# Optimization experiments

Hardware: AMD Instinct MI355X
Metric: run time of the kernel (lower is better)

## Reference

```python
import jax, jax.numpy as jnp
import numpy as np

BOS = 1
MAX_LEN = 20


def _lstm_cell(x, h, c, Wih, Whh, bih, bhh):
    # torch.nn.LSTMCell gate order: i, f, g, o
    g = x @ Wih.T + h @ Whh.T + bih + bhh
    i, f, gg, o = jnp.split(g, 4, axis=-1)
    c = jax.nn.sigmoid(f) * c + jax.nn.sigmoid(i) * jnp.tanh(gg)
    h = jax.nn.sigmoid(o) * jnp.tanh(c)
    return h, c


def setup_inputs() -> dict:
    key = jax.random.key(0)
    ks = jax.random.split(key, 12)
    B, K, D = 512, 36, 2048
    A, H, Em, V = 512, 512, 300, 10000
    s = 0.02
    rn = lambda k, shape, sc=s: sc * jax.random.normal(k, shape, dtype=jnp.float32)
    return {
        'feats': jax.random.normal(ks[0], (B, K, D), dtype=jnp.float32),
        'Wp': rn(ks[1], (A, D)), 'bp': jnp.zeros((A,), jnp.float32),
        'E': rn(ks[2], (V, Em), 0.1).at[0].set(0.0),  # padding_idx = 0
        'Wih1': rn(ks[3], (4 * H, Em + A)), 'Whh1': rn(ks[4], (4 * H, H)),
        'bih1': jnp.zeros((4 * H,), jnp.float32), 'bhh1': jnp.zeros((4 * H,), jnp.float32),
        'Wih2': rn(ks[5], (4 * H, H + A)), 'Whh2': rn(ks[6], (4 * H, H)),
        'bih2': jnp.zeros((4 * H,), jnp.float32), 'bhh2': jnp.zeros((4 * H,), jnp.float32),
        'Wa1': rn(ks[7], (A, H + A)), 'ba1': jnp.zeros((A,), jnp.float32),
        'wa2': rn(ks[8], (1, A)), 'ba2': jnp.zeros((1,), jnp.float32),
        'Wo': rn(ks[9], (V, H)), 'bo': jnp.zeros((V,), jnp.float32),
    }


def reference(feats, Wp, bp, E, Wih1, Whh1, bih1, bhh1, Wih2, Whh2, bih2, bhh2,
              Wa1, ba1, wa2, ba2, Wo, bo):
    B, K, D = feats.shape
    H = Whh1.shape[1]
    f_att = feats @ Wp.T + bp                      # [B, K, A]
    f_mean = f_att.mean(axis=1)                    # [B, A]
    # attn Linear over concat([h1, f_att]): split columns, precompute f_att term
    Wa1_h, Wa1_f = Wa1[:, :H], Wa1[:, H:]
    att_f = f_att @ Wa1_f.T + ba1                  # [B, K, A]
    x0 = jnp.broadcast_to(E[BOS], (B, E.shape[1]))
    z = jnp.zeros((B, H), jnp.float32)
    carry0 = (x0, z, z, z, z)

    def step(carry, _):
        x, h1, c1, h2, c2 = carry
        h1, c1 = _lstm_cell(jnp.concatenate([x, f_mean], axis=-1), h1, c1,
                            Wih1, Whh1, bih1, bhh1)
        pre = jnp.tanh(att_f + (h1 @ Wa1_h.T)[:, None, :])   # [B, K, A]
        e = pre @ wa2[0] + ba2[0]                            # [B, K]
        alpha = jax.nn.softmax(e, axis=-1)
        ctx = jnp.einsum('bk,bka->ba', alpha, f_att)         # [B, A]
        h2, c2 = _lstm_cell(jnp.concatenate([h1, ctx], axis=-1), h2, c2,
                            Wih2, Whh2, bih2, bhh2)
        logit = h2 @ Wo.T + bo                               # [B, V]  (dropout is identity in eval)
        nxt = jnp.argmax(logit, axis=-1)
        return (E[nxt], h1, c1, h2, c2), nxt

    _, ids = jax.lax.scan(step, carry0, None, length=MAX_LEN - 1)
    return ids.T  # [B, MAX_LEN-1], matches torch.stack(out_ids, 1)
```

## Files before the change

kernel.cpp:

```cpp
#include <hip/hip_runtime.h>
#include <math.h>
#include <stdint.h>

constexpr int Bsz = 512, Kf = 36, Dd = 2048, Aa = 512, Hh = 512, Em = 300;
constexpr int Vv = 10000, TSTEPS = 19, BOS = 1;
constexpr int K1 = 832;
constexpr int K2 = 1536;
constexpr int VvP = 10112;
constexpr int NTL = VvP / 64;
constexpr float SPLIT_S  = 2048.0f;
constexpr float SPLIT_IS = 1.0f / 2048.0f;

#define CDIV(a,b) (((a)+(b)-1)/(b))

typedef _Float16 f16x8 __attribute__((ext_vector_type(8)));
typedef float    f32x4 __attribute__((ext_vector_type(4)));

typedef const unsigned int GU __attribute__((address_space(1)));
typedef unsigned int       LU __attribute__((address_space(3)));

__device__ __forceinline__ void gload16(const void* g, void* l) {
    __builtin_amdgcn_global_load_lds((GU*)g, (LU*)l, 16, 0, 0);
}

template<int N> __device__ __forceinline__ void wait_vm() {
    if constexpr (N == 0)       asm volatile("s_waitcnt vmcnt(0)" ::: "memory");
    else if constexpr (N == 3)  asm volatile("s_waitcnt vmcnt(3)" ::: "memory");
    else if constexpr (N == 6)  asm volatile("s_waitcnt vmcnt(6)" ::: "memory");
    else if constexpr (N == 8)  asm volatile("s_waitcnt vmcnt(8)" ::: "memory");
    else static_assert(N == 0, "unsupported vmcnt literal");
}
#define WAIT_LGKM asm volatile("s_waitcnt lgkmcnt(0)" ::: "memory")
#define SB0 __builtin_amdgcn_sched_barrier(0)
#define BAR __builtin_amdgcn_s_barrier()

__device__ __forceinline__ float sigm(float v) { return 1.0f / (1.0f + expf(-v)); }

__device__ __forceinline__ void wsplit(_Float16* __restrict__ hi, _Float16* __restrict__ lo,
                                       size_t idx, float v) {
    _Float16 h = (_Float16)v;
    hi[idx] = h;
    lo[idx] = (_Float16)((v - (float)h) * SPLIT_S);
}


template<int BM, int BN, int BK, int WVM, int OCC, int EPI>
__global__ __launch_bounds__(256, OCC)
void gemm_sp(const _Float16* __restrict__ Ahi, const _Float16* __restrict__ Alo, int lda,
             const _Float16* __restrict__ Bhi, const _Float16* __restrict__ Blo, int ldb,
             float* __restrict__ C, int ldc, int N, int K,
             const float* __restrict__ bias1, const float* __restrict__ bias2,
             const float* __restrict__ addC,
             float* __restrict__ cbuf,
             _Float16* __restrict__ d1h, _Float16* __restrict__ d1l, int ld1, int off1,
             _Float16* __restrict__ d2h, _Float16* __restrict__ d2l, int ld2, int off2,
             float* __restrict__ candV, int* __restrict__ candI, int ntl)
{
    static_assert(EPI != 2 || WVM == 4, "LSTM epilogue needs 4x1 wave grid");
    constexpr int WVN = 4 / WVM;
    constexpr int WM = BM / WVM, WN = BN / WVN;
    constexpr int MF = WM / 16, NF = WN / 16;
    constexpr int PA  = BK / 8;
    constexpr int PSA = BM * 8 + 8;
    constexpr int PSB = BN * 8 + 8;
    constexpr int SZA = PA * PSA, SZB = PA * PSB;
    constexpr int OAH = 0, OAL = SZA, OBH = 2 * SZA, OBL = 2 * SZA + SZB;
    constexpr int BUF = 2 * SZA + 2 * SZB;
    constexpr int NCHA = BM * BK / 2048;
    constexpr int NCHB = BN * BK / 2048;
    constexpr int LW = 2 * NCHA + 2 * NCHB;
    __shared__ _Float16 sm[2 * BUF];

    const int nt = blockIdx.x, mt = blockIdx.y;
    const int m0 = mt * BM, n0 = nt * BN;

    const int t    = threadIdx.x;
    const int lane = t & 63;
    const int w    = t >> 6;
    const int wr   = w / WVN, wc = w % WVN;
    const int l15  = lane & 15, l4 = lane >> 4;

    f32x4 acch[MF][NF];
    f32x4 accm[MF][NF];
    #pragma unroll
    for (int m = 0; m < MF; ++m)
        #pragma unroll
        for (int n = 0; n < NF; ++n) {
            acch[m][n] = (f32x4){0.f, 0.f, 0.f, 0.f};
            accm[m][n] = (f32x4){0.f, 0.f, 0.f, 0.f};
        }

    const int nkt = K / BK;

    auto stage = [&](int bufo, int kt) {
        #pragma unroll
        for (int i = 0; i < NCHA; ++i) {
            const int q  = i * 256 + t;
            const int p  = q / BM, r = q % BM;
            const int qw = i * 256 + (t & ~63);
            const int pu = qw / BM, ru = qw % BM;
            const size_t goff = (size_t)(m0 + r) * lda + kt * BK + p * 8;
            gload16(Ahi + goff, &sm[bufo + OAH + pu * PSA + ru * 8]);
            gload16(Alo + goff, &sm[bufo + OAL + pu * PSA + ru * 8]);
        }
        #pragma unroll
        for (int i = 0; i < NCHB; ++i) {
            const int q  = i * 256 + t;
            const int p  = q / BN, r = q % BN;
            const int qw = i * 256 + (t & ~63);
            const int pu = qw / BN, ru = qw % BN;
            const size_t goff = (size_t)(n0 + r) * ldb + kt * BK + p * 8;
            gload16(Bhi + goff, &sm[bufo + OBH + pu * PSB + ru * 8]);
            gload16(Blo + goff, &sm[bufo + OBL + pu * PSB + ru * 8]);
// ... 112 lines not shown
                }
        #pragma unroll
        for (int mask = 1; mask < 16; mask <<= 1) {
            #pragma unroll
            for (int m = 0; m < MF; ++m)
                #pragma unroll
                for (int r = 0; r < 4; ++r) {
                    const float ov = __shfl_xor(bv[m][r], mask);
                    const int   oi = __shfl_xor(bix[m][r], mask);
                    if (ov > bv[m][r] || (ov == bv[m][r] && oi < bix[m][r])) {
                        bv[m][r] = ov; bix[m][r] = oi;
                    }
                }
        }
        __syncthreads();
        if (l15 == 0) {
            #pragma unroll
            for (int m = 0; m < MF; ++m)
                #pragma unroll
                for (int r = 0; r < 4; ++r) {
                    const int rl = wr * WM + m * 16 + l4 * 4 + r;
                    sEv[wc * BM + rl] = bv[m][r];
                    sEi[wc * BM + rl] = bix[m][r];
                }
        }
        __syncthreads();
        if (t < BM) {
            float v0 = sEv[t]; int i0 = sEi[t];
            const float v1 = sEv[BM + t]; const int i1 = sEi[BM + t];
            if (v1 > v0 || (v1 == v0 && i1 < i0)) { v0 = v1; i0 = i1; }
            candV[(size_t)(m0 + t) * ntl + nt] = v0;
            candI[(size_t)(m0 + t) * ntl + nt] = i0;
        }
    }
}

__global__ __launch_bounds__(512, 4)
void gemm_af32(const float* __restrict__ Af, int lda,
               const _Float16* __restrict__ Bhi, const _Float16* __restrict__ Blo, int ldb,
               float* __restrict__ C, int ldc, int N, int K,
               const float* __restrict__ bias1, int gxn)
{
    constexpr int BM = 128, BN = 64, BK = 32;
    constexpr int WM = 32, WN = 32;
    constexpr int MF = 2, NF = 2;
    constexpr int PSA = BM * 8 + 8;
    constexpr int PSB = BN * 8 + 8;
    constexpr int PA  = BK / 8;
    constexpr int SZA = PA * PSA, SZB = PA * PSB;
    constexpr int OAH = 0, OAL = SZA, OBH = 2 * SZA, OBL = 2 * SZA + SZB;
    constexpr int BUF = 2 * SZA + 2 * SZB;
    __shared__ _Float16 sm[2 * BUF];

    const int nwg = gridDim.x;
    const int cpx = nwg >> 3;
    const int orig = blockIdx.x;
    const int lid = (orig & 7) * cpx + (orig >> 3);
    const int nt = lid % gxn, mt = lid / gxn;
    const int m0 = mt * BM, n0 = nt * BN;

    const int t    = threadIdx.x;
    const int lane = t & 63;
    const int w    = t >> 6;
    const int wr   = w >> 1, wc = w & 1;
    const int l15  = lane & 15, l4 = lane >> 4;
    const int ar   = t >> 2, ac = t & 3;

    f32x4 acch[MF][NF];
    f32x4 accm[MF][NF];
    #pragma unroll
    for (int m = 0; m < MF; ++m)
        #pragma unroll
        for (int n = 0; n < NF; ++n) {
            acch[m][n] = (f32x4){0.f, 0.f, 0.f, 0.f};
            accm[m][n] = (f32x4){0.f, 0.f, 0.f, 0.f};
        }

    const int nkt = K / BK;

    auto issueA = [&](float4 (&rd)[2], int kt) {
        const float* src = Af + (size_t)(m0 + ar) * lda + kt * BK + ac * 8;
        rd[0] = *(const float4*)src;
        rd[1] = *(const float4*)(src + 4);
    };
    auto writeA = [&](int bufo, float4 (&rd)[2]) {
        const float f[8] = {rd[0].x, rd[0].y, rd[0].z, rd[0].w,
                            rd[1].x, rd[1].y, rd[1].z, rd[1].w};
        f16x8 hi, lo;
        #pragma unroll
        for (int j = 0; j < 8; ++j) {
            _Float16 h = (_Float16)f[j];
            hi[j] = h;
            lo[j] = (_Float16)((f[j] - (float)h) * SPLIT_S);
        }
        *(f16x8*)&sm[bufo + OAH + ac * PSA + ar * 8] = hi;
        *(f16x8*)&sm[bufo + OAL + ac * PSA + ar * 8] = lo;
    };
    auto stageB = [&](int bufo, int kt) {
        const int q = t & 255;
        const int p = q >> 6, r = q & 63;
        const _Float16* src = (t < 256) ? Bhi : Blo;
        const int base = (t < 256) ? (bufo + OBH) : (bufo + OBL);
        const size_t goff = (size_t)(n0 + r) * ldb + kt * BK + p * 8;
        gload16(src + goff, &sm[base + p * PSB + r * 8]);
    };
    auto compute = [&](int bufo) {
        f16x8 ah[MF], al[MF], bh[NF], bl[NF];
        const int pl = l4;
        #pragma unroll
        for (int m = 0; m < MF; ++m) {
            const int row = wr * WM + m * 16 + l15;
            ah[m] = *(const f16x8*)&sm[bufo + OAH + pl * PSA + row * 8];
            al[m] = *(const f16x8*)&sm[bufo + OAL + pl * PSA + row * 8];
        }
        #pragma unroll
        for (int n = 0; n < NF; ++n) {
            const int row = wc * WN + n * 16 + l15;
            bh[n] = *(const f16x8*)&sm[bufo + OBH + pl * PSB + row * 8];
            bl[n] = *(const f16x8*)&sm[bufo + OBL + pl * PSB + row * 8];
        }
        #pragma unroll
        for (int m = 0; m < MF; ++m)
            #pragma unroll
            for (int n = 0; n < NF; ++n) {
                acch[m][n] = __builtin_amdgcn_mfma_f32_16x16x32_f16(ah[m], bh[n], acch[m][n], 0, 0, 0);
                accm[m][n] = __builtin_amdgcn_mfma_f32_16x16x32_f16(ah[m], bl[n], accm[m][n], 0, 0, 0);
                accm[m][n] = __builtin_amdgcn_mfma_f32_16x16x32_f16(al[m], bh[n], accm[m][n], 0, 0, 0);
            }
    };

    float4 rA[2], rB[2];
    issueA(rA, 0); stageB(0, 0);
    for (int kt = 0; kt < nkt; kt += 2) {
        issueA(rB, kt + 1); stageB(BUF, kt + 1);
        wait_vm<3>(); SB0;
        writeA(0, rA);
        WAIT_LGKM; SB0;
        BAR; SB0;
        compute(0);
        SB0; WAIT_LGKM; BAR; SB0;
        if (kt + 2 < nkt) { issueA(rA, kt + 2); stageB(0, kt + 2); wait_vm<3>(); }
        else              { wait_vm<0>(); }
        SB0;
        writeA(BUF, rB);
        WAIT_LGKM; SB0;
        BAR; SB0;
        compute(BUF);
        SB0; WAIT_LGKM; BAR; SB0;
    }

    #pragma unroll
    for (int m = 0; m < MF; ++m) {
        const int rowb = m0 + wr * WM + m * 16 + l4 * 4;
        #pragma unroll
        for (int n = 0; n < NF; ++n) {
            const int col = n0 + wc * WN + n * 16 + l15;
            float bb = bias1 ? bias1[col] : 0.f;
            #pragma unroll
            for (int r = 0; r < 4; ++r) {
                const size_t idx = (size_t)(rowb + r) * ldc + col;
                C[idx] = acch[m][n][r] + accm[m][n][r] * SPLIT_IS + bb;
            }
        }
    }
}

__global__ __launch_bounds__(256)
void split_convert(const float* __restrict__ src, int srcld, int validR,
                   _Float16* __restrict__ dhi, _Float16* __restrict__ dlo,
                   int dstld, int coloff, int R, int C, int gperm)
{
    const int total = R * C;
    for (int i = blockIdx.x * 256 + threadIdx.x; i < total; i += gridDim.x * 256) {
        const int r = i / C, c = i % C;
        int dr = r;
        if (gperm) {
            const int gate = r >> 9, h = r & 511;
            dr = ((h >> 4) << 6) + (gate << 4) + (h & 15);
        }
        const float v = (r < validR) ? src[(size_t)r * srcld + c] : 0.f;
        wsplit(dhi, dlo, (size_t)dr * dstld + coloff + c, v);
    }
}

__global__ __launch_bounds__(256)
void init_kernel(_Float16* __restrict__ a1h0, _Float16* __restrict__ a1l0,
                 _Float16* __restrict__ a1h1, _Float16* __restrict__ a1l1,
                 _Float16* __restrict__ a2h0, _Float16* __restrict__ a2l0,
                 _Float16* __restrict__ a2h1, _Float16* __restrict__ a2l1,
                 float* __restrict__ c1, float* __restrict__ c2,
                 const float* __restrict__ E)
{
    const int idx = blockIdx.x * 256 + threadIdx.x;
    if (idx < Bsz * K1) {
        const int col = idx % K1;
        const float v = (col < Em) ? E[(size_t)BOS * Em + col] : 0.f;
        wsplit(a1h0, a1l0, idx, v);
        wsplit(a1h1, a1l1, idx, 0.f);
    }
    if (idx < Bsz * K2) {
        wsplit(a2h0, a2l0, idx, 0.f);
        wsplit(a2h1, a2l1, idx, 0.f);
    }
    if (idx < Bsz * Hh) { c1[idx] = 0.f; c2[idx] = 0.f; }
}

__global__ __launch_bounds__(256)
void fmean_kernel(const float* __restrict__ f_att, float* __restrict__ f_mean,
                  _Float16* __restrict__ fmh, _Float16* __restrict__ fml)
{
    const int b = blockIdx.x;
    for (int a = threadIdx.x; a < Aa; a += 256) {
        float s = 0.f;
        for (int k = 0; k < Kf; ++k) s += f_att[((size_t)b * Kf + k) * Aa + a];
        const float v = s * (1.0f / 36.0f);
        f_mean[(size_t)b * Aa + a] = v;
        wsplit(fmh, fml, (size_t)b * Aa + a, v);
    }
}

__global__ __launch_bounds__(256)
void attn_fused(const float* __restrict__ att_f, const float* __restrict__ q,
                const float* __restrict__ wa2, const float* __restrict__ ba2,
                const float* __restrict__ f_att,
                _Float16* __restrict__ a2h, _Float16* __restrict__ a2l)
{
    const int b = blockIdx.x, tid = threadIdx.x;
    const int w = tid >> 6, lane = tid & 63;
    __shared__ float se[Kf];
    __shared__ float wk[Kf];
    const float* pq = q + (size_t)b * Aa;
    for (int k = w; k < Kf; k += 4) {
        const float* pf = att_f + ((size_t)b * Kf + k) * Aa;
        float s = 0.f;
        #pragma unroll
        for (int j = 0; j < Aa; j += 64) {
            const int a = j + lane;
            s += tanhf(pf[a] + pq[a]) * wa2[a];
        }
        #pragma unroll
        for (int off = 32; off; off >>= 1) s += __shfl_down(s, off);
        if (lane == 0) se[k] = s + ba2[0];
    }
    __syncthreads();
    if (tid < Kf) {
        float mx = -INFINITY;
        for (int k = 0; k < Kf; ++k) mx = fmaxf(mx, se[k]);
        float ssum = 0.f;
        for (int k = 0; k < Kf; ++k) ssum += expf(se[k] - mx);
        wk[tid] = expf(se[tid] - mx) / ssum;
    }
    __syncthreads();
    for (int a = tid; a < Aa; a += 256) {
        float acc = 0.f;
        for (int k = 0; k < Kf; ++k)
            acc = fmaf(wk[k], f_att[((size_t)b * Kf + k) * Aa + a], acc);
        wsplit(a2h, a2l, (size_t)b * K2 + Hh + a, acc);
    }
}

__global__ __launch_bounds__(256)
void argmax_embed_kernel(const float* __restrict__ candV, const int* __restrict__ candI,
                         const float* __restrict__ E,
                         _Float16* __restrict__ a1h, _Float16* __restrict__ a1l,
                         int* __restrict__ out, int t, int ntl)
{
    const int b = blockIdx.x;
    const int tid = threadIdx.x;
    __shared__ float sv[256];
    __shared__ int   si[256];
    float bvv = -INFINITY; int bii = 0x7fffffff;
    if (tid < ntl) { bvv = candV[(size_t)b * ntl + tid]; bii = candI[(size_t)b * ntl + tid]; }
    sv[tid] = bvv; si[tid] = bii;
    __syncthreads();
    for (int s = 128; s > 0; s >>= 1) {
        if (tid < s) {
            const float v2 = sv[tid + s];
            const int   i2 = si[tid + s];
            if (v2 > sv[tid] || (v2 == sv[tid] && i2 < si[tid])) { sv[tid] = v2; si[tid] = i2; }
        }
        __syncthreads();
    }
    const int idx = si[0];
    if (tid == 0) out[(size_t)b * TSTEPS + t] = idx;
    for (int d = tid; d < Em; d += 256)
        wsplit(a1h, a1l, (size_t)b * K1 + d, E[(size_t)idx * Em + d]);
}

static inline void conv(hipStream_t s, const float* src, int srcld, int validR,
                        _Float16* dhi, _Float16* dlo, int dstld, int coloff,
                        int R, int C, int gperm)
{
    int blocks = CDIV(R * C, 256); if (blocks > 2048) blocks = 2048;
    split_convert<<<dim3(blocks), dim3(256), 0, s>>>(src, srcld, validR, dhi, dlo,
                                                     dstld, coloff, R, C, gperm);
}

extern "C" void kernel_launch(void* const* d_in, const int* in_sizes, int n_in,
                              void* d_out, int out_size, void* d_ws, size_t ws_size,
                              hipStream_t stream)
{
    const float* feats = (const float*)d_in[0];
    const float* Wp    = (const float*)d_in[1];
    const float* bp    = (const float*)d_in[2];
    const float* E     = (const float*)d_in[3];
    const float* Wih1  = (const float*)d_in[4];
    const float* Whh1  = (const float*)d_in[5];
    const float* bih1  = (const float*)d_in[6];
    const float* bhh1  = (const float*)d_in[7];
    const float* Wih2  = (const float*)d_in[8];
    const float* Whh2  = (const float*)d_in[9];
    const float* bih2  = (const float*)d_in[10];
    const float* bhh2  = (const float*)d_in[11];
    const float* Wa1   = (const float*)d_in[12];
    const float* ba1   = (const float*)d_in[13];
    const float* wa2   = (const float*)d_in[14];
    const float* ba2   = (const float*)d_in[15];
    const float* Wo    = (const float*)d_in[16];
    const float* bo    = (const float*)d_in[17];
    int* out = (int*)d_out;
    (void)in_sizes; (void)n_in; (void)out_size; (void)ws_size;

    uint8_t* w = (uint8_t*)d_ws;
    size_t off = 0;
    auto alloc = [&](size_t bytes) { void* p = w + off; off = (off + bytes + 255) & ~(size_t)255; return p; };

    float*     f_att  = (float*)alloc(18432ull * 512 * 4);
    float*     att_f  = (float*)alloc(18432ull * 512 * 4);
    float*     f_mean = (float*)alloc(512ull * 512 * 4);
    _Float16*  fmh    = (_Float16*)alloc(512ull * 512 * 2);
    _Float16*  fml    = (_Float16*)alloc(512ull * 512 * 2);
    _Float16*  wph    = (_Float16*)alloc(512ull * 2048 * 2);
    _Float16*  wpl    = (_Float16*)alloc(512ull * 2048 * 2);
    _Float16*  w1ph   = (_Float16*)alloc(2048ull * K1 * 2);
    _Float16*  w1pl   = (_Float16*)alloc(2048ull * K1 * 2);
    _Float16*  w1ch   = (_Float16*)alloc(2048ull * 512 * 2);
    _Float16*  w1cl   = (_Float16*)alloc(2048ull * 512 * 2);
    _Float16*  w2ph   = (_Float16*)alloc(2048ull * K2 * 2);
    _Float16*  w2pl   = (_Float16*)alloc(2048ull * K2 * 2);
    _Float16*  wahh   = (_Float16*)alloc(512ull * 512 * 2);
    _Float16*  wahl   = (_Float16*)alloc(512ull * 512 * 2);
    _Float16*  wafh   = (_Float16*)alloc(512ull * 512 * 2);
    _Float16*  wafl   = (_Float16*)alloc(512ull * 512 * 2);
    _Float16*  woh    = (_Float16*)alloc((size_t)VvP * 512 * 2);
    _Float16*  wol    = (_Float16*)alloc((size_t)VvP * 512 * 2);
    float*     g1c    = (float*)alloc(512ull * 2048 * 4);
    _Float16*  a1h[2] = {(_Float16*)alloc(512ull * K1 * 2), (_Float16*)alloc(512ull * K1 * 2)};
    _Float16*  a1l[2] = {(_Float16*)alloc(512ull * K1 * 2), (_Float16*)alloc(512ull * K1 * 2)};
    _Float16*  a2h[2] = {(_Float16*)alloc(512ull * K2 * 2), (_Float16*)alloc(512ull * K2 * 2)};
    _Float16*  a2l[2] = {(_Float16*)alloc(512ull * K2 * 2), (_Float16*)alloc(512ull * K2 * 2)};
    float*     c1     = (float*)alloc(512ull * 512 * 4);
    float*     c2     = (float*)alloc(512ull * 512 * 4);
    float*     qbuf   = (float*)alloc(512ull * 512 * 4);
    float*     candV  = (float*)alloc(512ull * NTL * 4);
    int*       candI  = (int*)alloc(512ull * NTL * 4);

    conv(stream, Wp,        Dd,      512,  wph,  wpl,  2048, 0,    512,  2048, 0);
    conv(stream, Wih1,      Em + Aa, 2048, w1ph, w1pl, K1,   0,    2048, Em,   1);
    conv(stream, Whh1,      Hh,      2048, w1ph, w1pl, K1,   Em,   2048, 512,  1);
    conv(stream, Wih1,      Em + Aa, 0,    w1ph, w1pl, K1,   812,  2048, 20,   1);
    conv(stream, Wih1 + Em, Em + Aa, 2048, w1ch, w1cl, 512,  0,    2048, 512,  1);
    conv(stream, Wih2,      Hh + Aa, 2048, w2ph, w2pl, K2,   0,    2048, 1024, 1);
    conv(stream, Whh2,      Hh,      2048, w2ph, w2pl, K2,   1024, 2048, 512,  1);
    conv(stream, Wa1,       Hh + Aa, 512,  wahh, wahl, 512,  0,    512,  512,  0);
    conv(stream, Wa1 + Hh,  Hh + Aa, 512,  wafh, wafl, 512,  0,    512,  512,  0);
    conv(stream, Wo,        Hh,      Vv,   woh,  wol,  512,  0,    VvP,  512,  0);

    init_kernel<<<dim3(CDIV(Bsz * K2, 256)), dim3(256), 0, stream>>>(
        a1h[0], a1l[0], a1h[1], a1l[1], a2h[0], a2l[0], a2h[1], a2l[1], c1, c2, E);

    gemm_af32<<<dim3(1152), dim3(512), 0, stream>>>(
        feats, Dd, wph, wpl, 2048, f_att, 512, 512, 2048, bp, 8);
    fmean_kernel<<<dim3(Bsz), dim3(256), 0, stream>>>(f_att, f_mean, fmh, fml);
    gemm_sp<64, 64, 64, 2, 1, 1><<<dim3(32, 8), 256, 0, stream>>>(
        fmh, fml, 512, w1ch, w1cl, 512, g1c, 2048, 2048, 512,
        bih1, bhh1, nullptr,
        nullptr, nullptr, nullptr, 0, 0, nullptr, nullptr, 0, 0, nullptr, nullptr, 0);
    gemm_af32<<<dim3(1152), dim3(512), 0, stream>>>(
        f_att, 512, wafh, wafl, 512, att_f, 512, 512, 512, ba1, 8);

    for (int t = 0; t < TSTEPS; ++t) {
        const int cur = t & 1, nxt = cur ^ 1;
        gemm_sp<64, 64, 64, 4, 2, 2><<<dim3(32, 8), 256, 0, stream>>>(
            a1h[cur], a1l[cur], K1, w1ph, w1pl, K1, nullptr, 2048, 2048, K1,
            nullptr, nullptr, g1c,
            c1, a2h[cur], a2l[cur], K2, 0, a1h[nxt], a1l[nxt], K1, Em,
            nullptr, nullptr, 0);
        gemm_sp<64, 64, 64, 2, 1, 0><<<dim3(8, 8), 256, 0, stream>>>(
            a2h[cur], a2l[cur], K2, wahh, wahl, 512, qbuf, 512, 512, 512,
            nullptr, nullptr, nullptr,
            nullptr, nullptr, nullptr, 0, 0, nullptr, nullptr, 0, 0, nullptr, nullptr, 0);
        attn_fused<<<dim3(Bsz), dim3(256), 0, stream>>>(
            att_f, qbuf, wa2, ba2, f_att, a2h[cur], a2l[cur]);
        gemm_sp<64, 64, 64, 4, 2, 2><<<dim3(32, 8), 256, 0, stream>>>(
            a2h[cur], a2l[cur], K2, w2ph, w2pl, K2, nullptr, 2048, 2048, K2,
            bih2, bhh2, nullptr,
            c2, a2h[nxt], a2l[nxt], K2, 1024, nullptr, nullptr, 0, 0,
            nullptr, nullptr, 0);
        gemm_sp<64, 64, 64, 2, 1, 3><<<dim3(NTL, 8), 256, 0, stream>>>(
            a2h[nxt] + 1024, a2l[nxt] + 1024, K2, woh, wol, 512, nullptr, 0, Vv, 512,
            bo, nullptr, nullptr,
            nullptr, nullptr, nullptr, 0, 0, nullptr, nullptr, 0, 0, candV, candI, NTL);
        argmax_embed_kernel<<<dim3(Bsz), dim3(256), 0, stream>>>(
            candV, candI, E, a1h[nxt], a1l[nxt], out, t, NTL);
    }
}
```

Baseline: 3.394 ms.

## Fuse decode loop into one persistent kernel with software grid barriers

Replaces the 19×6 per-step kernel launches with a single persistent kernel of 512 blocks that runs every decode stage and separates stages with an atomic-counter grid barrier. The aim is to remove launch and inter-kernel gap overhead across the many small serial steps. In exchange, the barriers cost spinning and atomics, only part of the blocks work in some stages, and correctness relies on all 512 blocks being co-resident (launch bounds allow 2 per CU). Occupancy is also capped by the shared-memory and launch-bounds settings.

```diff
diff --git a/kernel.cpp b/kernel.cpp
--- a/kernel.cpp
+++ b/kernel.cpp
@@ -8,6 +8,7 @@
 constexpr int K2 = 1536;
 constexpr int VvP = 10112;
 constexpr int NTL = VvP / 64;
+constexpr int NBLK = 512;
 constexpr float SPLIT_S  = 2048.0f;
 constexpr float SPLIT_IS = 1.0f / 2048.0f;
 
@@ -44,17 +45,40 @@
 }
 
 
-template<int BM, int BN, int BK, int WVM, int OCC, int EPI>
-__global__ __launch_bounds__(256, OCC)
-void gemm_sp(const _Float16* __restrict__ Ahi, const _Float16* __restrict__ Alo, int lda,
-             const _Float16* __restrict__ Bhi, const _Float16* __restrict__ Blo, int ldb,
-             float* __restrict__ C, int ldc, int N, int K,
-             const float* __restrict__ bias1, const float* __restrict__ bias2,
-             const float* __restrict__ addC,
-             float* __restrict__ cbuf,
-             _Float16* __restrict__ d1h, _Float16* __restrict__ d1l, int ld1, int off1,
-             _Float16* __restrict__ d2h, _Float16* __restrict__ d2l, int ld2, int off2,
-             float* __restrict__ candV, int* __restrict__ candI, int ntl)
+constexpr int SMEM64 = 2 * (2 * 8 * (64 * 8 + 8) + 2 * 8 * (64 * 8 + 8));
+
+__device__ __forceinline__ void gbar(unsigned* cnt, unsigned* sns, unsigned& ls) {
+    __syncthreads();
+    if (threadIdx.x == 0) {
+        const unsigned next = ls + 1;
+        __threadfence();
+        const unsigned prev = __hip_atomic_fetch_add(cnt, 1u, __ATOMIC_ACQ_REL,
+                                                     __HIP_MEMORY_SCOPE_AGENT);
+        if (prev == (unsigned)NBLK - 1) {
+            __hip_atomic_store(cnt, 0u, __ATOMIC_RELAXED, __HIP_MEMORY_SCOPE_AGENT);
+            __hip_atomic_store(sns, next, __ATOMIC_RELEASE, __HIP_MEMORY_SCOPE_AGENT);
+        } else {
+            while (__hip_atomic_load(sns, __ATOMIC_ACQUIRE,
+                                     __HIP_MEMORY_SCOPE_AGENT) < next)
+                __builtin_amdgcn_s_sleep(8);
+        }
+        ls = next;
+    }
+    __syncthreads();
+}
+
+template<int BM, int BN, int BK, int WVM, int EPI>
+__device__ void gemm_dev(
+    _Float16* __restrict__ sm, int mt, int nt,
+    const _Float16* __restrict__ Ahi, const _Float16* __restrict__ Alo, int lda,
+    const _Float16* __restrict__ Bhi, const _Float16* __restrict__ Blo, int ldb,
+    float* __restrict__ C, int ldc, int N, int K,
+    const float* __restrict__ bias1, const float* __restrict__ bias2,
+    const float* __restrict__ addC,
+    float* __restrict__ cbuf,
+    _Float16* __restrict__ d1h, _Float16* __restrict__ d1l, int ld1, int off1,
+    _Float16* __restrict__ d2h, _Float16* __restrict__ d2l, int ld2, int off2,
+    float* __restrict__ candV, int* __restrict__ candI, int ntl)
 {
     static_assert(EPI != 2 || WVM == 4, "LSTM epilogue needs 4x1 wave grid");
     constexpr int WVN = 4 / WVM;
@@ -69,16 +93,15 @@
     constexpr int NCHA = BM * BK / 2048;
     constexpr int NCHB = BN * BK / 2048;
     constexpr int LW = 2 * NCHA + 2 * NCHB;
-    __shared__ _Float16 sm[2 * BUF];
-
-    const int nt = blockIdx.x, mt = blockIdx.y;
+
     const int m0 = mt * BM, n0 = nt * BN;
-
     const int t    = threadIdx.x;
     const int lane = t & 63;
     const int w    = t >> 6;
     const int wr   = w / WVN, wc = w % WVN;
     const int l15  = lane & 15, l4 = lane >> 4;
+
+    __syncthreads();
 
     f32x4 acch[MF][NF];
     f32x4 accm[MF][NF];
@@ -260,6 +283,152 @@
     }
 }
 
+template<int BM, int BN, int BK, int WVM, int EPI>
+__global__ __launch_bounds__(256, 2)
+void gemm16(const _Float16* __restrict__ Ahi, const _Float16* __restrict__ Alo, int lda,
+            const _Float16* __restrict__ Bhi, const _Float16* __restrict__ Blo, int ldb,
+            float* __restrict__ C, int ldc, int N, int K,
+            const float* __restrict__ bias1, const float* __restrict__ bias2)
+{
+    __shared__ _Float16 sm[SMEM64];
+    gemm_dev<BM, BN, BK, WVM, EPI>(sm, blockIdx.y, blockIdx.x,
+        Ahi, Alo, lda, Bhi, Blo, ldb, C, ldc, N, K,
+        bias1, bias2, nullptr,
+        nullptr, nullptr, nullptr, 0, 0, nullptr, nullptr, 0, 0,
+        nullptr, nullptr, 0);
+}
+
+__device__ void attn_dev(_Float16* smbase, int b,
+                         const float* __restrict__ att_f, const float* __restrict__ q,
+                         const float* __restrict__ wa2, const float* __restrict__ ba2,
+                         const float* __restrict__ f_att,
+                         _Float16* __restrict__ a2h, _Float16* __restrict__ a2l)
+{
+    float* se = reinterpret_cast<float*>(smbase);
+    float* wk = se + Kf;
+    const int tid = threadIdx.x;
+    const int w = tid >> 6, lane = tid & 63;
+    __syncthreads();
+    const float* pq = q + (size_t)b * Aa;
+    for (int k = w; k < Kf; k += 4) {
+        const float* pf = att_f + ((size_t)b * Kf + k) * Aa;
+        float s = 0.f;
+        #pragma unroll
+        for (int j = 0; j < Aa; j += 64) {
+            const int a = j + lane;
+            s += tanhf(pf[a] + pq[a]) * wa2[a];
+        }
+        #pragma unroll
+        for (int off = 32; off; off >>= 1) s += __shfl_down(s, off);
+        if (lane == 0) se[k] = s + ba2[0];
+    }
+    __syncthreads();
+    if (tid < Kf) {
+        float mx = -INFINITY;
+        for (int k = 0; k < Kf; ++k) mx = fmaxf(mx, se[k]);
+        float ssum = 0.f;
+        for (int k = 0; k < Kf; ++k) ssum += expf(se[k] - mx);
+        wk[tid] = expf(se[tid] - mx) / ssum;
+    }
+    __syncthreads();
+    for (int a = tid; a < Aa; a += 256) {
+        float acc = 0.f;
+        for (int k = 0; k < Kf; ++k)
+            acc = fmaf(wk[k], f_att[((size_t)b * Kf + k) * Aa + a], acc);
+        wsplit(a2h, a2l, (size_t)b * K2 + Hh + a, acc);
+    }
+}
+
+__device__ void argmax_dev(_Float16* smbase, int b,
+                           const float* __restrict__ candV, const int* __restrict__ candI,
+                           const float* __restrict__ E,
+                           _Float16* __restrict__ a1h, _Float16* __restrict__ a1l,
+                           int* __restrict__ out, int t, int ntl)
+{
+    float* sv = reinterpret_cast<float*>(smbase);
+    int*   si = reinterpret_cast<int*>(sv + 256);
+    const int tid = threadIdx.x;
+    __syncthreads();
+    float bvv = -INFINITY; int bii = 0x7fffffff;
+    if (tid < ntl) { bvv = candV[(size_t)b * ntl + tid]; bii = candI[(size_t)b * ntl + tid]; }
+    sv[tid] = bvv; si[tid] = bii;
+    __syncthreads();
+    for (int s = 128; s > 0; s >>= 1) {
+        if (tid < s) {
+            const float v2 = sv[tid + s];
+            const int   i2 = si[tid + s];
+            if (v2 > sv[tid] || (v2 == sv[tid] && i2 < si[tid])) { sv[tid] = v2; si[tid] = i2; }
+        }
+        __syncthreads();
+    }
+    const int idx = si[0];
+    if (tid == 0) out[(size_t)b * TSTEPS + t] = idx;
+    for (int d = tid; d < Em; d += 256)
+        wsplit(a1h, a1l, (size_t)b * K1 + d, E[(size_t)idx * Em + d]);
+}
+
+struct DecodeArgs {
+    _Float16 *a1h0, *a1l0, *a1h1, *a1l1;
+    _Float16 *a2h0, *a2l0, *a2h1, *a2l1;
+    const _Float16 *w1ph, *w1pl, *w2ph, *w2pl, *wahh, *wahl, *woh, *wol;
+    const float *g1c, *bih2, *bhh2, *bo, *wa2, *ba2, *att_f, *f_att, *E;
+    float *c1, *c2, *qbuf, *candV;
+    int *candI, *outp;
+    unsigned *barCnt, *barSns;
+};
+
+__global__ __launch_bounds__(256, 2)
+void decode_loop(DecodeArgs A)
+{
+    __shared__ _Float16 sm[SMEM64];
+    const int blk = blockIdx.x;
+    unsigned ls = 0;
+    _Float16* a1h[2] = {A.a1h0, A.a1h1};
+    _Float16* a1l[2] = {A.a1l0, A.a1l1};
+    _Float16* a2h[2] = {A.a2h0, A.a2h1};
+    _Float16* a2l[2] = {A.a2l0, A.a2l1};
+
+    for (int t = 0; t < TSTEPS; ++t) {
+        const int cur = t & 1, nxt = cur ^ 1;
+        if (blk < 256)
+            gemm_dev<64, 64, 64, 4, 2>(sm, blk >> 5, blk & 31,
+                a1h[cur], a1l[cur], K1, A.w1ph, A.w1pl, K1,
+                nullptr, 2048, 2048, K1,
+                nullptr, nullptr, A.g1c,
+                A.c1, a2h[cur], a2l[cur], K2, 0, a1h[nxt], a1l[nxt], K1, Em,
+                nullptr, nullptr, 0);
+        gbar(A.barCnt, A.barSns, ls);
+        if (blk < 64)
+            gemm_dev<64, 64, 64, 2, 0>(sm, blk >> 3, blk & 7,
+                a2h[cur], a2l[cur], K2, A.wahh, A.wahl, 512,
+                A.qbuf, 512, 512, 512,
+                nullptr, nullptr, nullptr,
+                nullptr, nullptr, nullptr, 0, 0, nullptr, nullptr, 0, 0,
+                nullptr, nullptr, 0);
+        gbar(A.barCnt, A.barSns, ls);
+        attn_dev(sm, blk, A.att_f, A.qbuf, A.wa2, A.ba2, A.f_att, a2h[cur], a2l[cur]);
+        gbar(A.barCnt, A.barSns, ls);
+        if (blk < 256)
+            gemm_dev<64, 64, 64, 4, 2>(sm, blk >> 5, blk & 31,
+                a2h[cur], a2l[cur], K2, A.w2ph, A.w2pl, K2,
+                nullptr, 2048, 2048, K2,
+                A.bih2, A.bhh2, nullptr,
+                A.c2, a2h[nxt], a2l[nxt], K2, 1024, nullptr, nullptr, 0, 0,
+                nullptr, nullptr, 0);
+        gbar(A.barCnt, A.barSns, ls);
+        for (int j = blk; j < 8 * NTL; j += NBLK)
+            gemm_dev<64, 64, 64, 2, 3>(sm, j / NTL, j % NTL,
+                a2h[nxt] + 1024, a2l[nxt] + 1024, K2, A.woh, A.wol, 512,
+                nullptr, 0, Vv, 512,
+                A.bo, nullptr, nullptr,
+                nullptr, nullptr, nullptr, 0, 0, nullptr, nullptr, 0, 0,
+                A.candV, A.candI, NTL);
+        gbar(A.barCnt, A.barSns, ls);
+        argmax_dev(sm, blk, A.candV, A.candI, A.E, a1h[nxt], a1l[nxt], A.outp, t, NTL);
+        gbar(A.barCnt, A.barSns, ls);
+    }
+}
+
 __global__ __launch_bounds__(512, 4)
 void gemm_af32(const float* __restrict__ Af, int lda,
                const _Float16* __restrict__ Bhi, const _Float16* __restrict__ Blo, int ldb,
@@ -414,6 +583,7 @@
                  _Float16* __restrict__ a2h0, _Float16* __restrict__ a2l0,
                  _Float16* __restrict__ a2h1, _Float16* __restrict__ a2l1,
                  float* __restrict__ c1, float* __restrict__ c2,
+                 unsigned* __restrict__ bar,
                  const float* __restrict__ E)
 {
     const int idx = blockIdx.x * 256 + threadIdx.x;
@@ -428,6 +598,7 @@
         wsplit(a2h1, a2l1, idx, 0.f);
     }
     if (idx < Bsz * Hh) { c1[idx] = 0.f; c2[idx] = 0.f; }
+    if (idx < 2) bar[idx] = 0u;
 }
 
 __global__ __launch_bounds__(256)
@@ -442,74 +613,6 @@
         f_mean[(size_t)b * Aa + a] = v;
         wsplit(fmh, fml, (size_t)b * Aa + a, v);
     }
-}
-
-__global__ __launch_bounds__(256)
-void attn_fused(const float* __restrict__ att_f, const float* __restrict__ q,
-                const float* __restrict__ wa2, const float* __restrict__ ba2,
-                const float* __restrict__ f_att,
-                _Float16* __restrict__ a2h, _Float16* __restrict__ a2l)
-{
-    const int b = blockIdx.x, tid = threadIdx.x;
-    const int w = tid >> 6, lane = tid & 63;
-    __shared__ float se[Kf];
-    __shared__ float wk[Kf];
-    const float* pq = q + (size_t)b * Aa;
-    for (int k = w; k < Kf; k += 4) {
-        const float* pf = att_f + ((size_t)b * Kf + k) * Aa;
-        float s = 0.f;
-        #pragma unroll
-        for (int j = 0; j < Aa; j += 64) {
-            const int a = j + lane;
-            s += tanhf(pf[a] + pq[a]) * wa2[a];
-        }
-        #pragma unroll
-        for (int off = 32; off; off >>= 1) s += __shfl_down(s, off);
-        if (lane == 0) se[k] = s + ba2[0];
-    }
-    __syncthreads();
-    if (tid < Kf) {
-        float mx = -INFINITY;
-        for (int k = 0; k < Kf; ++k) mx = fmaxf(mx, se[k]);
-        float ssum = 0.f;
-        for (int k = 0; k < Kf; ++k) ssum += expf(se[k] - mx);
-        wk[tid] = expf(se[tid] - mx) / ssum;
-    }
-    __syncthreads();
-    for (int a = tid; a < Aa; a += 256) {
-        float acc = 0.f;
-        for (int k = 0; k < Kf; ++k)
-            acc = fmaf(wk[k], f_att[((size_t)b * Kf + k) * Aa + a], acc);
-        wsplit(a2h, a2l, (size_t)b * K2 + Hh + a, acc);
-    }
-}
-
-__global__ __launch_bounds__(256)
-void argmax_embed_kernel(const float* __restrict__ candV, const int* __restrict__ candI,
-                         const float* __restrict__ E,
-                         _Float16* __restrict__ a1h, _Float16* __restrict__ a1l,
-                         int* __restrict__ out, int t, int ntl)
-{
-    const int b = blockIdx.x;
-    const int tid = threadIdx.x;
-    __shared__ float sv[256];
-    __shared__ int   si[256];
-    float bvv = -INFINITY; int bii = 0x7fffffff;
-    if (tid < ntl) { bvv = candV[(size_t)b * ntl + tid]; bii = candI[(size_t)b * ntl + tid]; }
-    sv[tid] = bvv; si[tid] = bii;
-    __syncthreads();
-    for (int s = 128; s > 0; s >>= 1) {
-        if (tid < s) {
-            const float v2 = sv[tid + s];
-            const int   i2 = si[tid + s];
-            if (v2 > sv[tid] || (v2 == sv[tid] && i2 < si[tid])) { sv[tid] = v2; si[tid] = i2; }
-        }
-        __syncthreads();
-    }
-    const int idx = si[0];
-    if (tid == 0) out[(size_t)b * TSTEPS + t] = idx;
-    for (int d = tid; d < Em; d += 256)
-        wsplit(a1h, a1l, (size_t)b * K1 + d, E[(size_t)idx * Em + d]);
 }
 
 static inline void conv(hipStream_t s, const float* src, int srcld, int validR,
@@ -579,6 +682,7 @@
     float*     qbuf   = (float*)alloc(512ull * 512 * 4);
     float*     candV  = (float*)alloc(512ull * NTL * 4);
     int*       candI  = (int*)alloc(512ull * NTL * 4);
+    unsigned*  barSt  = (unsigned*)alloc(256);
 
     conv(stream, Wp,        Dd,      512,  wph,  wpl,  2048, 0,    512,  2048, 0);
     conv(stream, Wih1,      Em + Aa, 2048, w1ph, w1pl, K1,   0,    2048, Em,   1);
@@ -592,41 +696,26 @@
     conv(stream, Wo,        Hh,      Vv,   woh,  wol,  512,  0,    VvP,  512,  0);
 
     init_kernel<<<dim3(CDIV(Bsz * K2, 256)), dim3(256), 0, stream>>>(
-        a1h[0], a1l[0], a1h[1], a1l[1], a2h[0], a2l[0], a2h[1], a2l[1], c1, c2, E);
+        a1h[0], a1l[0], a1h[1], a1l[1], a2h[0], a2l[0], a2h[1], a2l[1],
+        c1, c2, barSt, E);
 
     gemm_af32<<<dim3(1152), dim3(512), 0, stream>>>(
         feats, Dd, wph, wpl, 2048, f_att, 512, 512, 2048, bp, 8);
     fmean_kernel<<<dim3(Bsz), dim3(256), 0, stream>>>(f_att, f_mean, fmh, fml);
-    gemm_sp<64, 64, 64, 2, 1, 1><<<dim3(32, 8), 256, 0, stream>>>(
-        fmh, fml, 512, w1ch, w1cl, 512, g1c, 2048, 2048, 512,
-        bih1, bhh1, nullptr,
-        nullptr, nullptr, nullptr, 0, 0, nullptr, nullptr, 0, 0, nullptr, nullptr, 0);
+    gemm16<64, 64, 64, 2, 1><<<dim3(32, 8), 256, 0, stream>>>(
+        fmh, fml, 512, w1ch, w1cl, 512, g1c, 2048, 2048, 512, bih1, bhh1);
     gemm_af32<<<dim3(1152), dim3(512), 0, stream>>>(
         f_att, 512, wafh, wafl, 512, att_f, 512, 512, 512, ba1, 8);
 
-    for (int t = 0; t < TSTEPS; ++t) {
-        const int cur = t & 1, nxt = cur ^ 1;
-        gemm_sp<64, 64, 64, 4, 2, 2><<<dim3(32, 8), 256, 0, stream>>>(
-            a1h[cur], a1l[cur], K1, w1ph, w1pl, K1, nullptr, 2048, 2048, K1,
-            nullptr, nullptr, g1c,
-            c1, a2h[cur], a2l[cur], K2, 0, a1h[nxt], a1l[nxt], K1, Em,
-            nullptr, nullptr, 0);
-        gemm_sp<64, 64, 64, 2, 1, 0><<<dim3(8, 8), 256, 0, stream>>>(
-            a2h[cur], a2l[cur], K2, wahh, wahl, 512, qbuf, 512, 512, 512,
-            nullptr, nullptr, nullptr,
-            nullptr, nullptr, nullptr, 0, 0, nullptr, nullptr, 0, 0, nullptr, nullptr, 0);
-        attn_fused<<<dim3(Bsz), dim3(256), 0, stream>>>(
-            att_f, qbuf, wa2, ba2, f_att, a2h[cur], a2l[cur]);
-        gemm_sp<64, 64, 64, 4, 2, 2><<<dim3(32, 8), 256, 0, stream>>>(
-            a2h[cur], a2l[cur], K2, w2ph, w2pl, K2, nullptr, 2048, 2048, K2,
-            bih2, bhh2, nullptr,
-            c2, a2h[nxt], a2l[nxt], K2, 1024, nullptr, nullptr, 0, 0,
-            nullptr, nullptr, 0);
-        gemm_sp<64, 64, 64, 2, 1, 3><<<dim3(NTL, 8), 256, 0, stream>>>(
-            a2h[nxt] + 1024, a2l[nxt] + 1024, K2, woh, wol, 512, nullptr, 0, Vv, 512,
-            bo, nullptr, nullptr,
-            nullptr, nullptr, nullptr, 0, 0, nullptr, nullptr, 0, 0, candV, candI, NTL);
-        argmax_embed_kernel<<<dim3(Bsz), dim3(256), 0, stream>>>(
-            candV, candI, E, a1h[nxt], a1l[nxt], out, t, NTL);
-    }
-}
+    DecodeArgs da;
+    da.a1h0 = a1h[0]; da.a1l0 = a1l[0]; da.a1h1 = a1h[1]; da.a1l1 = a1l[1];
+    da.a2h0 = a2h[0]; da.a2l0 = a2l[0]; da.a2h1 = a2h[1]; da.a2l1 = a2l[1];
+    da.w1ph = w1ph; da.w1pl = w1pl; da.w2ph = w2ph; da.w2pl = w2pl;
+    da.wahh = wahh; da.wahl = wahl; da.woh = woh; da.wol = wol;
+    da.g1c = g1c; da.bih2 = bih2; da.bhh2 = bhh2; da.bo = bo;
+    da.wa2 = wa2; da.ba2 = ba2; da.att_f = att_f; da.f_att = f_att; da.E = E;
+    da.c1 = c1; da.c2 = c2; da.qbuf = qbuf; da.candV = candV;
+    da.candI = candI; da.outp = out;
+    da.barCnt = barSt; da.barSns = barSt + 1;
+    decode_loop<<<dim3(NBLK), dim3(256), 0, stream>>>(da);
+}
```

After: 13.32 ms. +292.4%, slower.

## Fuse final argmax and embedding lookup into vocab GEMM via last-block counter

Applied to the files above, without the earlier changes.

Drops the separate argmax_embed kernel. The vocab-projection GEMM now uses an atomic per-row-tile counter, so the last finishing block reduces the candidate maxima, writes the output ids, and scatters the split-fp16 embeddings for the next step. This removes one launch per timestep and the associated tail bubble, at the cost of a serialized reduction in a single block per row tile plus a threadfence and atomic in every block. It also raises gemm_af32 launch-bounds occupancy from 4 to 6.

```diff
diff --git a/kernel.cpp b/kernel.cpp
--- a/kernel.cpp
+++ b/kernel.cpp
@@ -54,7 +54,9 @@
              float* __restrict__ cbuf,
              _Float16* __restrict__ d1h, _Float16* __restrict__ d1l, int ld1, int off1,
              _Float16* __restrict__ d2h, _Float16* __restrict__ d2l, int ld2, int off2,
-             float* __restrict__ candV, int* __restrict__ candI, int ntl)
+             float* __restrict__ candV, int* __restrict__ candI, int ntl,
+             unsigned* __restrict__ cnt, const float* __restrict__ Eemb,
+             int* __restrict__ outp, int tstep)
 {
     static_assert(EPI != 2 || WVM == 4, "LSTM epilogue needs 4x1 wave grid");
     constexpr int WVN = 4 / WVM;
@@ -257,10 +259,54 @@
             candV[(size_t)(m0 + t) * ntl + nt] = v0;
             candI[(size_t)(m0 + t) * ntl + nt] = i0;
         }
-    }
-}
-
-__global__ __launch_bounds__(512, 4)
+        __threadfence();
+        __syncthreads();
+        __shared__ int sDone;
+        if (t == 0) {
+            const unsigned prev = __hip_atomic_fetch_add(cnt + mt, 1u,
+                                    __ATOMIC_ACQ_REL, __HIP_MEMORY_SCOPE_AGENT);
+            sDone = (prev == (unsigned)ntl - 1);
+            if (sDone) __hip_atomic_store(cnt + mt, 0u, __ATOMIC_RELAXED,
+                                          __HIP_MEMORY_SCOPE_AGENT);
+        }
+        __syncthreads();
+        if (!sDone) return;
+        float* sV = reinterpret_cast<float*>(&sm[0]);
+        int*   sI = reinterpret_cast<int*>(sV + 256);
+        int*   sIdx = sI + 256;
+        const int rl = t & 63, part = t >> 6;
+        const int b = m0 + rl;
+        float fv = -INFINITY; int fi = 0x7fffffff;
+        const int j0 = part * ((ntl + 3) >> 2);
+        const int j1 = min(ntl, j0 + ((ntl + 3) >> 2));
+        for (int j = j0; j < j1; ++j) {
+            const float v2 = candV[(size_t)b * ntl + j];
+            const int   i2 = candI[(size_t)b * ntl + j];
+            if (v2 > fv || (v2 == fv && i2 < fi)) { fv = v2; fi = i2; }
+        }
+        sV[t] = fv; sI[t] = fi;
+        __syncthreads();
+        if (t < 64) {
+            float v0 = sV[t]; int i0 = sI[t];
+            #pragma unroll
+            for (int p2 = 1; p2 < 4; ++p2) {
+                const float v2 = sV[t + p2 * 64];
+                const int   i2 = sI[t + p2 * 64];
+                if (v2 > v0 || (v2 == v0 && i2 < i0)) { v0 = v2; i0 = i2; }
+            }
+            outp[(size_t)(m0 + t) * TSTEPS + tstep] = i0;
+            sIdx[t] = i0;
+        }
+        __syncthreads();
+        for (int i = t; i < 64 * Em; i += 256) {
+            const int bb = i / Em, d = i % Em;
+            wsplit(d1h, d1l, (size_t)(m0 + bb) * ld1 + d,
+                   Eemb[(size_t)sIdx[bb] * Em + d]);
+        }
+    }
+}
+
+__global__ __launch_bounds__(512, 6)
 void gemm_af32(const float* __restrict__ Af, int lda,
                const _Float16* __restrict__ Bhi, const _Float16* __restrict__ Blo, int ldb,
                float* __restrict__ C, int ldc, int N, int K,
@@ -414,6 +460,7 @@
                  _Float16* __restrict__ a2h0, _Float16* __restrict__ a2l0,
                  _Float16* __restrict__ a2h1, _Float16* __restrict__ a2l1,
                  float* __restrict__ c1, float* __restrict__ c2,
+                 unsigned* __restrict__ cnt,
                  const float* __restrict__ E)
 {
     const int idx = blockIdx.x * 256 + threadIdx.x;
@@ -428,6 +475,7 @@
         wsplit(a2h1, a2l1, idx, 0.f);
     }
     if (idx < Bsz * Hh) { c1[idx] = 0.f; c2[idx] = 0.f; }
+    if (idx < 8) cnt[idx] = 0u;
 }
 
 __global__ __launch_bounds__(256)
@@ -482,34 +530,6 @@
             acc = fmaf(wk[k], f_att[((size_t)b * Kf + k) * Aa + a], acc);
         wsplit(a2h, a2l, (size_t)b * K2 + Hh + a, acc);
     }
-}
-
-__global__ __launch_bounds__(256)
-void argmax_embed_kernel(const float* __restrict__ candV, const int* __restrict__ candI,
-                         const float* __restrict__ E,
-                         _Float16* __restrict__ a1h, _Float16* __restrict__ a1l,
-                         int* __restrict__ out, int t, int ntl)
-{
-    const int b = blockIdx.x;
-    const int tid = threadIdx.x;
-    __shared__ float sv[256];
-    __shared__ int   si[256];
-    float bvv = -INFINITY; int bii = 0x7fffffff;
-    if (tid < ntl) { bvv = candV[(size_t)b * ntl + tid]; bii = candI[(size_t)b * ntl + tid]; }
-    sv[tid] = bvv; si[tid] = bii;
-    __syncthreads();
-    for (int s = 128; s > 0; s >>= 1) {
-        if (tid < s) {
-            const float v2 = sv[tid + s];
-            const int   i2 = si[tid + s];
-            if (v2 > sv[tid] || (v2 == sv[tid] && i2 < si[tid])) { sv[tid] = v2; si[tid] = i2; }
-        }
-        __syncthreads();
-    }
-    const int idx = si[0];
-    if (tid == 0) out[(size_t)b * TSTEPS + t] = idx;
-    for (int d = tid; d < Em; d += 256)
-        wsplit(a1h, a1l, (size_t)b * K1 + d, E[(size_t)idx * Em + d]);
 }
 
 static inline void conv(hipStream_t s, const float* src, int srcld, int validR,
@@ -579,6 +599,7 @@
     float*     qbuf   = (float*)alloc(512ull * 512 * 4);
     float*     candV  = (float*)alloc(512ull * NTL * 4);
     int*       candI  = (int*)alloc(512ull * NTL * 4);
+    unsigned*  cntArr = (unsigned*)alloc(256);
 
     conv(stream, Wp,        Dd,      512,  wph,  wpl,  2048, 0,    512,  2048, 0);
     conv(stream, Wih1,      Em + Aa, 2048, w1ph, w1pl, K1,   0,    2048, Em,   1);
@@ -592,7 +613,8 @@
     conv(stream, Wo,        Hh,      Vv,   woh,  wol,  512,  0,    VvP,  512,  0);
 
     init_kernel<<<dim3(CDIV(Bsz * K2, 256)), dim3(256), 0, stream>>>(
-        a1h[0], a1l[0], a1h[1], a1l[1], a2h[0], a2l[0], a2h[1], a2l[1], c1, c2, E);
+        a1h[0], a1l[0], a1h[1], a1l[1], a2h[0], a2l[0], a2h[1], a2l[1],
+        c1, c2, cntArr, E);
 
     gemm_af32<<<dim3(1152), dim3(512), 0, stream>>>(
         feats, Dd, wph, wpl, 2048, f_att, 512, 512, 2048, bp, 8);
@@ -600,7 +622,8 @@
     gemm_sp<64, 64, 64, 2, 1, 1><<<dim3(32, 8), 256, 0, stream>>>(
         fmh, fml, 512, w1ch, w1cl, 512, g1c, 2048, 2048, 512,
         bih1, bhh1, nullptr,
-        nullptr, nullptr, nullptr, 0, 0, nullptr, nullptr, 0, 0, nullptr, nullptr, 0);
+        nullptr, nullptr, nullptr, 0, 0, nullptr, nullptr, 0, 0,
+        nullptr, nullptr, 0, nullptr, nullptr, nullptr, 0);
     gemm_af32<<<dim3(1152), dim3(512), 0, stream>>>(
         f_att, 512, wafh, wafl, 512, att_f, 512, 512, 512, ba1, 8);
 
@@ -610,23 +633,23 @@
             a1h[cur], a1l[cur], K1, w1ph, w1pl, K1, nullptr, 2048, 2048, K1,
             nullptr, nullptr, g1c,
             c1, a2h[cur], a2l[cur], K2, 0, a1h[nxt], a1l[nxt], K1, Em,
-            nullptr, nullptr, 0);
+            nullptr, nullptr, 0, nullptr, nullptr, nullptr, 0);
         gemm_sp<64, 64, 64, 2, 1, 0><<<dim3(8, 8), 256, 0, stream>>>(
             a2h[cur], a2l[cur], K2, wahh, wahl, 512, qbuf, 512, 512, 512,
             nullptr, nullptr, nullptr,
-            nullptr, nullptr, nullptr, 0, 0, nullptr, nullptr, 0, 0, nullptr, nullptr, 0);
+            nullptr, nullptr, nullptr, 0, 0, nullptr, nullptr, 0, 0,
+            nullptr, nullptr, 0, nullptr, nullptr, nullptr, 0);
         attn_fused<<<dim3(Bsz), dim3(256), 0, stream>>>(
             att_f, qbuf, wa2, ba2, f_att, a2h[cur], a2l[cur]);
         gemm_sp<64, 64, 64, 4, 2, 2><<<dim3(32, 8), 256, 0, stream>>>(
             a2h[cur], a2l[cur], K2, w2ph, w2pl, K2, nullptr, 2048, 2048, K2,
             bih2, bhh2, nullptr,
             c2, a2h[nxt], a2l[nxt], K2, 1024, nullptr, nullptr, 0, 0,
-            nullptr, nullptr, 0);
+            nullptr, nullptr, 0, nullptr, nullptr, nullptr, 0);
         gemm_sp<64, 64, 64, 2, 1, 3><<<dim3(NTL, 8), 256, 0, stream>>>(
             a2h[nxt] + 1024, a2l[nxt] + 1024, K2, woh, wol, 512, nullptr, 0, Vv, 512,
             bo, nullptr, nullptr,
-            nullptr, nullptr, nullptr, 0, 0, nullptr, nullptr, 0, 0, candV, candI, NTL);
-        argmax_embed_kernel<<<dim3(Bsz), dim3(256), 0, stream>>>(
-            candV, candI, E, a1h[nxt], a1l[nxt], out, t, NTL);
-    }
-}
+            nullptr, a1h[nxt], a1l[nxt], K1, 0, nullptr, nullptr, 0, 0,
+            candV, candI, NTL, cntArr, E, out, t);
+    }
+}
```

Measured after the change: 6.956 ms. +105.0%, slower.

## Pre-split feats into fp16 hi/lo and stage A via async LDS loads

Applied to the files above, without the earlier changes.

Adds a separate pass that splits the fp32 feats tensor into fp16 hi/lo arrays, and makes the big projection GEMM load both A halves with direct global-to-LDS loads instead of register loads with in-kernel conversion. The first GEMM also writes a hi/lo split of f_att, so the second GEMM reads pre-split input. The goal is to remove register staging and conversion from the GEMM main loop and simplify its pipeline. The cost is an extra full pass over feats plus fp16 traffic: reading 151MB of fp32 and writing 151MB of fp16, then reading that 151MB back in the GEMM, versus reading 151MB once before.

```diff
diff --git a/kernel.cpp b/kernel.cpp
--- a/kernel.cpp
+++ b/kernel.cpp
@@ -260,11 +260,13 @@
     }
 }
 
+template<int PAIR>
 __global__ __launch_bounds__(512, 4)
-void gemm_af32(const float* __restrict__ Af, int lda,
-               const _Float16* __restrict__ Bhi, const _Float16* __restrict__ Blo, int ldb,
-               float* __restrict__ C, int ldc, int N, int K,
-               const float* __restrict__ bias1, int gxn)
+void gemm_sp512(const _Float16* __restrict__ Ahi, const _Float16* __restrict__ Alo, int lda,
+                const _Float16* __restrict__ Bhi, const _Float16* __restrict__ Blo, int ldb,
+                float* __restrict__ C, int ldc, int N, int K,
+                const float* __restrict__ bias1, int gxn,
+                _Float16* __restrict__ pairH, _Float16* __restrict__ pairL)
 {
     constexpr int BM = 128, BN = 64, BK = 32;
     constexpr int WM = 32, WN = 32;
@@ -289,7 +291,6 @@
     const int w    = t >> 6;
     const int wr   = w >> 1, wc = w & 1;
     const int l15  = lane & 15, l4 = lane >> 4;
-    const int ar   = t >> 2, ac = t & 3;
 
     f32x4 acch[MF][NF];
     f32x4 accm[MF][NF];
@@ -303,31 +304,21 @@
 
     const int nkt = K / BK;
 
-    auto issueA = [&](float4 (&rd)[2], int kt) {
-        const float* src = Af + (size_t)(m0 + ar) * lda + kt * BK + ac * 8;
-        rd[0] = *(const float4*)src;
-        rd[1] = *(const float4*)(src + 4);
-    };
-    auto writeA = [&](int bufo, float4 (&rd)[2]) {
-        const float f[8] = {rd[0].x, rd[0].y, rd[0].z, rd[0].w,
-                            rd[1].x, rd[1].y, rd[1].z, rd[1].w};
-        f16x8 hi, lo;
-        #pragma unroll
-        for (int j = 0; j < 8; ++j) {
-            _Float16 h = (_Float16)f[j];
-            hi[j] = h;
-            lo[j] = (_Float16)((f[j] - (float)h) * SPLIT_S);
-        }
-        *(f16x8*)&sm[bufo + OAH + ac * PSA + ar * 8] = hi;
-        *(f16x8*)&sm[bufo + OAL + ac * PSA + ar * 8] = lo;
-    };
-    auto stageB = [&](int bufo, int kt) {
-        const int q = t & 255;
-        const int p = q >> 6, r = q & 63;
-        const _Float16* src = (t < 256) ? Bhi : Blo;
-        const int base = (t < 256) ? (bufo + OBH) : (bufo + OBL);
-        const size_t goff = (size_t)(n0 + r) * ldb + kt * BK + p * 8;
-        gload16(src + goff, &sm[base + p * PSB + r * 8]);
+    auto stage = [&](int bufo, int kt) {
+        {
+            const int p = t >> 7, r = t & 127;
+            const size_t goff = (size_t)(m0 + r) * lda + kt * BK + p * 8;
+            gload16(Ahi + goff, &sm[bufo + OAH + p * PSA + r * 8]);
+            gload16(Alo + goff, &sm[bufo + OAL + p * PSA + r * 8]);
+        }
+        {
+            const int q = t & 255;
+            const int p = q >> 6, r = q & 63;
+            const _Float16* src = (t < 256) ? Bhi : Blo;
+            const int base = (t < 256) ? (bufo + OBH) : (bufo + OBL);
+            const size_t goff = (size_t)(n0 + r) * ldb + kt * BK + p * 8;
+            gload16(src + goff, &sm[base + p * PSB + r * 8]);
+        }
     };
     auto compute = [&](int bufo) {
         f16x8 ah[MF], al[MF], bh[NF], bl[NF];
@@ -354,23 +345,14 @@
             }
     };
 
-    float4 rA[2], rB[2];
-    issueA(rA, 0); stageB(0, 0);
-    for (int kt = 0; kt < nkt; kt += 2) {
-        issueA(rB, kt + 1); stageB(BUF, kt + 1);
-        wait_vm<3>(); SB0;
-        writeA(0, rA);
-        WAIT_LGKM; SB0;
-        BAR; SB0;
-        compute(0);
-        SB0; WAIT_LGKM; BAR; SB0;
-        if (kt + 2 < nkt) { issueA(rA, kt + 2); stageB(0, kt + 2); wait_vm<3>(); }
+    stage(0, 0);
+    for (int kt = 0; kt < nkt; ++kt) {
+        const int bc = (kt & 1) * BUF;
+        if (kt + 1 < nkt) { stage(BUF - bc, kt + 1); wait_vm<3>(); }
         else              { wait_vm<0>(); }
         SB0;
-        writeA(BUF, rB);
-        WAIT_LGKM; SB0;
         BAR; SB0;
-        compute(BUF);
+        compute(bc);
         SB0; WAIT_LGKM; BAR; SB0;
     }
 
@@ -384,9 +366,31 @@
             #pragma unroll
             for (int r = 0; r < 4; ++r) {
                 const size_t idx = (size_t)(rowb + r) * ldc + col;
-                C[idx] = acch[m][n][r] + accm[m][n][r] * SPLIT_IS + bb;
+                const float v = acch[m][n][r] + accm[m][n][r] * SPLIT_IS + bb;
+                C[idx] = v;
+                if constexpr (PAIR) wsplit(pairH, pairL, idx, v);
             }
         }
+    }
+}
+
+__global__ __launch_bounds__(256)
+void split_flat8(const float* __restrict__ src,
+                 _Float16* __restrict__ dh, _Float16* __restrict__ dl, int n8)
+{
+    for (int i = blockIdx.x * 256 + threadIdx.x; i < n8; i += gridDim.x * 256) {
+        const float4 a = ((const float4*)src)[2 * i];
+        const float4 b = ((const float4*)src)[2 * i + 1];
+        const float f[8] = {a.x, a.y, a.z, a.w, b.x, b.y, b.z, b.w};
+        f16x8 hi, lo;
+        #pragma unroll
+        for (int j = 0; j < 8; ++j) {
+            _Float16 h = (_Float16)f[j];
+            hi[j] = h;
+            lo[j] = (_Float16)((f[j] - (float)h) * SPLIT_S);
+        }
+        ((f16x8*)dh)[i] = hi;
+        ((f16x8*)dl)[i] = lo;
     }
 }
 
@@ -552,6 +556,10 @@
 
     float*     f_att  = (float*)alloc(18432ull * 512 * 4);
     float*     att_f  = (float*)alloc(18432ull * 512 * 4);
+    _Float16*  fth    = (_Float16*)alloc(18432ull * 2048 * 2);
+    _Float16*  ftl    = (_Float16*)alloc(18432ull * 2048 * 2);
+    _Float16*  fah    = (_Float16*)alloc(18432ull * 512 * 2);
+    _Float16*  fal    = (_Float16*)alloc(18432ull * 512 * 2);
     float*     f_mean = (float*)alloc(512ull * 512 * 4);
     _Float16*  fmh    = (_Float16*)alloc(512ull * 512 * 2);
     _Float16*  fml    = (_Float16*)alloc(512ull * 512 * 2);
@@ -590,19 +598,21 @@
     conv(stream, Wa1,       Hh + Aa, 512,  wahh, wahl, 512,  0,    512,  512,  0);
     conv(stream, Wa1 + Hh,  Hh + Aa, 512,  wafh, wafl, 512,  0,    512,  512,  0);
     conv(stream, Wo,        Hh,      Vv,   woh,  wol,  512,  0,    VvP,  512,  0);
+    split_flat8<<<dim3(2048), dim3(256), 0, stream>>>(feats, fth, ftl, 18432 * 2048 / 8);
 
     init_kernel<<<dim3(CDIV(Bsz * K2, 256)), dim3(256), 0, stream>>>(
         a1h[0], a1l[0], a1h[1], a1l[1], a2h[0], a2l[0], a2h[1], a2l[1], c1, c2, E);
 
-    gemm_af32<<<dim3(1152), dim3(512), 0, stream>>>(
-        feats, Dd, wph, wpl, 2048, f_att, 512, 512, 2048, bp, 8);
+    gemm_sp512<1><<<dim3(1152), dim3(512), 0, stream>>>(
+        fth, ftl, Dd, wph, wpl, 2048, f_att, 512, 512, 2048, bp, 8, fah, fal);
     fmean_kernel<<<dim3(Bsz), dim3(256), 0, stream>>>(f_att, f_mean, fmh, fml);
     gemm_sp<64, 64, 64, 2, 1, 1><<<dim3(32, 8), 256, 0, stream>>>(
         fmh, fml, 512, w1ch, w1cl, 512, g1c, 2048, 2048, 512,
         bih1, bhh1, nullptr,
         nullptr, nullptr, nullptr, 0, 0, nullptr, nullptr, 0, 0, nullptr, nullptr, 0);
-    gemm_af32<<<dim3(1152), dim3(512), 0, stream>>>(
-        f_att, 512, wafh, wafl, 512, att_f, 512, 512, 512, ba1, 8);
+    gemm_sp512<0><<<dim3(1152), dim3(512), 0, stream>>>(
+        fah, fal, 512, wafh, wafl, 512, att_f, 512, 512, 512, ba1, 8,
+        nullptr, nullptr);
 
     for (int t = 0; t < TSTEPS; ++t) {
         const int cur = t & 1, nxt = cur ^ 1;
```

Result: slower. 3.548 ms (+4.5%).
